# Kernel optimization log

Hardware: AMD Instinct MI355X
Metric: run time of the kernel (lower is better)

## Reference

```python
import jax, jax.numpy as jnp
import numpy as np
from jax import lax

KSIZE = 11
SIGMA = 1.5
C1 = (0.01 * 1.0) ** 2
C2 = (0.03 * 1.0) ** 2
PAD = (KSIZE - 1) // 2  # 5


def _gaussian_2d(ksize: int, sigma: float) -> np.ndarray:
    half = (ksize - 1) * 0.5
    g = np.exp(-0.5 * (np.linspace(-half, half, ksize) / sigma) ** 2)
    g = g / g.sum()
    return np.outer(g, g).astype(np.float32)  # [k, k]


def setup_inputs() -> dict:
    key = jax.random.key(0)
    kx, ky = jax.random.split(key)
    B, C, T, H, W = 2, 3, 8, 512, 512
    x = jax.random.uniform(kx, (B, C, T, H, W), dtype=jnp.float32)
    y = jax.random.uniform(ky, (B, C, T, H, W), dtype=jnp.float32)
    k2d = jnp.asarray(_gaussian_2d(KSIZE, SIGMA))
    # depthwise conv3d kernel: [C_out=C, C_in/groups=1, kD=1, kH, kW]
    kernel = jnp.broadcast_to(k2d[None, None, None], (C, 1, 1, KSIZE, KSIZE))
    return {"x": x, "y": y, "kernel": kernel}


def reference(x, y, kernel):
    C = x.shape[1]

    def conv(z):
        return lax.conv_general_dilated(
            z, kernel,
            window_strides=(1, 1, 1),
            padding=((0, 0), (PAD, PAD), (PAD, PAD)),
            dimension_numbers=("NCDHW", "OIDHW", "NCDHW"),
            feature_group_count=C,
        )

    # single grouped conv over the 5 stacked statistics, as in the original
    stacked = jnp.concatenate([x, y, x * x, y * y, x * y], axis=0)
    ux, uy, uxx, uyy, uxy = jnp.split(conv(stacked), 5, axis=0)

    vx = uxx - ux * ux
    vy = uyy - uy * uy
    vxy = uxy - ux * uy
    a1 = 2.0 * ux * uy + C1
    a2 = 2.0 * vxy + C2
    b1 = ux * ux + uy * uy + C1
    b2 = vx + vy + C2
    return a1 * a2 / (b1 * b2)
```

## Files before the change

### kernel.cpp

```cpp
#include <hip/hip_runtime.h>
#include <type_traits>

namespace {
constexpr int HH = 512;
constexpr int WW = 512;
constexpr int KS = 11;
constexpr int PADR = 5;
constexpr int TH = 32;
constexpr int TW = 64;
constexpr int HC = TW + 2 * PADR;
constexpr int LP = 76;
constexpr int NTHREADS = 256;
constexpr float SSIM_C1 = 1.0e-4f;
constexpr float SSIM_C2 = 9.0e-4f;
}

__global__ __launch_bounds__(NTHREADS, 3) void ssim_fused(
    const float* __restrict__ x, const float* __restrict__ y,
    const float* __restrict__ kern, float* __restrict__ out)
{
    __shared__ __align__(16) float vb[5][TH][LP];

    constexpr int tiles_w = WW / TW;
    constexpr int tiles_h = HH / TH;
    constexpr int tpp = tiles_w * tiles_h;

    const int bid = blockIdx.x;
    const int plane = bid / tpp;
    const int trem = bid - plane * tpp;
    const int tr_idx = trem / tiles_w;
    const int tile_r = tr_idx * TH;
    const int tile_c = (trem - tr_idx * tiles_w) * TW;

    const float* __restrict__ xp = x + (size_t)plane * (HH * WW);
    const float* __restrict__ yp = y + (size_t)plane * (HH * WW);
    float* __restrict__ op = out + (size_t)plane * (HH * WW);

    float wt[KS];
    {
        const float c = kern[5 * KS + 5];
        const float inv = rsqrtf(c);
#pragma unroll
        for (int i = 0; i < KS; ++i) wt[i] = kern[5 * KS + i] * inv;
    }

    const int t = threadIdx.x;
    const bool interior = (tile_r >= PADR) && (tile_r + TH + PADR <= HH) &&
                          (tile_c >= PADR) && (tile_c + TW + PADR <= WW);

    auto phase1 = [&](auto intr_tag) {
        constexpr bool INTR = decltype(intr_tag)::value;
        for (int i = t; i < TH * HC; i += NTHREADS) {
            const int r = i / HC;
            const int c = i - r * HC;
            const int gr = tile_r + r;
            const int gc = tile_c + c - PADR;
            float sx = 0.f, sy = 0.f, sxx = 0.f, syy = 0.f, sxy = 0.f;
            if (INTR) {
                const float* xq = xp + (size_t)(gr - PADR) * WW + gc;
                const float* yq = yp + (size_t)(gr - PADR) * WW + gc;
#pragma unroll
                for (int k = 0; k < KS; ++k) {
                    const float xv = xq[(size_t)k * WW];
                    const float yv = yq[(size_t)k * WW];
                    const float w = wt[k];
                    sx  += w * xv;
                    sy  += w * yv;
                    sxx += w * xv * xv;
                    syy += w * yv * yv;
                    sxy += w * xv * yv;
                }
            } else {
                const bool cok = (gc >= 0) & (gc < WW);
#pragma unroll
                for (int k = 0; k < KS; ++k) {
                    const int rr = gr - PADR + k;
                    const bool ok = cok & (rr >= 0) & (rr < HH);
                    float xv = 0.f, yv = 0.f;
                    if (ok) {
                        xv = xp[(size_t)rr * WW + gc];
                        yv = yp[(size_t)rr * WW + gc];
                    }
                    const float w = wt[k];
                    sx  += w * xv;
                    sy  += w * yv;
                    sxx += w * xv * xv;
                    syy += w * yv * yv;
                    sxy += w * xv * yv;
                }
            }
            vb[0][r][c] = sx;
            vb[1][r][c] = sy;
            vb[2][r][c] = sxx;
            vb[3][r][c] = syy;
            vb[4][r][c] = sxy;
        }
    };

    if (interior) phase1(std::true_type{});
    else          phase1(std::false_type{});

    __syncthreads();

#pragma unroll
    for (int gi = 0; gi < (TH * (TW / 4)) / NTHREADS; ++gi) {
        const int g = t + gi * NTHREADS;
        const int r = g >> 4;
        const int c0 = (g & 15) * 4;
        float res[5][4];
#pragma unroll
        for (int s = 0; s < 5; ++s) {
            float wnd[KS + 3];
#pragma unroll
            for (int i2 = 0; i2 < KS + 3; ++i2) wnd[i2] = vb[s][r][c0 + i2];
#pragma unroll
            for (int j = 0; j < 4; ++j) {
                float a = 0.f;
#pragma unroll
                for (int k = 0; k < KS; ++k) a += wt[k] * wnd[j + k];
                res[s][j] = a;
            }
        }
        float4 o;
#pragma unroll
        for (int j = 0; j < 4; ++j) {
            const float ux = res[0][j], uy = res[1][j];
            const float uxx = res[2][j], uyy = res[3][j], uxy = res[4][j];
            const float vx  = uxx - ux * ux;
            const float vy  = uyy - uy * uy;
            const float vxy = uxy - ux * uy;
            const float a1 = 2.f * ux * uy + SSIM_C1;
            const float a2 = 2.f * vxy + SSIM_C2;
            const float b1 = ux * ux + uy * uy + SSIM_C1;
            const float b2 = vx + vy + SSIM_C2;
            (&o.x)[j] = (a1 * a2) * __builtin_amdgcn_rcpf(b1 * b2);
        }
        *(float4*)(op + (size_t)(tile_r + r) * WW + (tile_c + c0)) = o;
    }
}

extern "C" void kernel_launch(void* const* d_in, const int* in_sizes, int n_in,
                              void* d_out, int out_size, void* d_ws, size_t ws_size,
                              hipStream_t stream) {
    const float* x    = (const float*)d_in[0];
    const float* y    = (const float*)d_in[1];
    const float* kern = (const float*)d_in[2];
    float* out = (float*)d_out;

    const int nplanes = in_sizes[0] / (HH * WW);
    const int nblocks = nplanes * (HH / TH) * (WW / TW);

    ssim_fused<<<dim3(nblocks), dim3(NTHREADS), 0, stream>>>(x, y, kern, out);
}
```

Measured before the change: 229.6 us.

## Restructure SSIM into full-width row bands with register-sliding vertical window

New measurement: 368.8 us. 60.6% more time.

```diff
diff --git a/kernel.cpp b/kernel.cpp
--- a/kernel.cpp
+++ b/kernel.cpp
@@ -1,36 +1,31 @@
 #include <hip/hip_runtime.h>
 #include <type_traits>
 
+typedef float v2f __attribute__((ext_vector_type(2)));
+
 namespace {
-constexpr int HH = 512;
-constexpr int WW = 512;
-constexpr int KS = 11;
-constexpr int PADR = 5;
-constexpr int TH = 32;
-constexpr int TW = 64;
-constexpr int HC = TW + 2 * PADR;
-constexpr int LP = 76;
-constexpr int NTHREADS = 256;
+constexpr int HH = 512, WW = 512;
+constexpr int KS = 11, PADR = 5;
+constexpr int BH = 32;
+constexpr int SR = 4;
+constexpr int NSLAB = BH / SR;
+constexpr int WIN = SR + 2*PADR;
+constexpr int PITCH = 528;
+constexpr int NT = 256;
 constexpr float SSIM_C1 = 1.0e-4f;
 constexpr float SSIM_C2 = 9.0e-4f;
 }
 
-__global__ __launch_bounds__(NTHREADS, 3) void ssim_fused(
+__global__ __launch_bounds__(NT, 3) void ssim_fused(
     const float* __restrict__ x, const float* __restrict__ y,
     const float* __restrict__ kern, float* __restrict__ out)
 {
-    __shared__ __align__(16) float vb[5][TH][LP];
-
-    constexpr int tiles_w = WW / TW;
-    constexpr int tiles_h = HH / TH;
-    constexpr int tpp = tiles_w * tiles_h;
+    __shared__ __align__(16) float vb[5][SR][PITCH];
 
     const int bid = blockIdx.x;
-    const int plane = bid / tpp;
-    const int trem = bid - plane * tpp;
-    const int tr_idx = trem / tiles_w;
-    const int tile_r = tr_idx * TH;
-    const int tile_c = (trem - tr_idx * tiles_w) * TW;
+    const int plane = bid >> 4;
+    const int band = bid & 15;
+    const int R0 = band << 5;
 
     const float* __restrict__ xp = x + (size_t)plane * (HH * WW);
     const float* __restrict__ yp = y + (size_t)plane * (HH * WW);
@@ -38,105 +33,157 @@
 
     float wt[KS];
     {
-        const float c = kern[5 * KS + 5];
-        const float inv = rsqrtf(c);
+        const float inv = rsqrtf(kern[5 * KS + 5]);
 #pragma unroll
         for (int i = 0; i < KS; ++i) wt[i] = kern[5 * KS + i] * inv;
     }
 
     const int t = threadIdx.x;
-    const bool interior = (tile_r >= PADR) && (tile_r + TH + PADR <= HH) &&
-                          (tile_c >= PADR) && (tile_c + TW + PADR <= WW);
-
-    auto phase1 = [&](auto intr_tag) {
-        constexpr bool INTR = decltype(intr_tag)::value;
-        for (int i = t; i < TH * HC; i += NTHREADS) {
-            const int r = i / HC;
-            const int c = i - r * HC;
-            const int gr = tile_r + r;
-            const int gc = tile_c + c - PADR;
-            float sx = 0.f, sy = 0.f, sxx = 0.f, syy = 0.f, sxy = 0.f;
-            if (INTR) {
-                const float* xq = xp + (size_t)(gr - PADR) * WW + gc;
-                const float* yq = yp + (size_t)(gr - PADR) * WW + gc;
-#pragma unroll
-                for (int k = 0; k < KS; ++k) {
-                    const float xv = xq[(size_t)k * WW];
-                    const float yv = yq[(size_t)k * WW];
-                    const float w = wt[k];
-                    sx  += w * xv;
-                    sy  += w * yv;
-                    sxx += w * xv * xv;
-                    syy += w * yv * yv;
-                    sxy += w * xv * yv;
-                }
-            } else {
-                const bool cok = (gc >= 0) & (gc < WW);
-#pragma unroll
-                for (int k = 0; k < KS; ++k) {
-                    const int rr = gr - PADR + k;
-                    const bool ok = cok & (rr >= 0) & (rr < HH);
-                    float xv = 0.f, yv = 0.f;
-                    if (ok) {
-                        xv = xp[(size_t)rr * WW + gc];
-                        yv = yp[(size_t)rr * WW + gc];
+    const int c2 = 2 * t;
+    const int q  = t & 127;
+    const int rb = (t >> 7) * 2;
+
+    for (int i = t; i < 5 * SR * 16; i += NT) {
+        const int st = i >> 6;
+        const int rem = i & 63;
+        const int r = rem >> 4;
+        const int j = rem & 15;
+        vb[st][r][(j < 8) ? j : (512 + j)] = 0.f;
+    }
+
+    auto body = [&](auto edge_tag) {
+        constexpr bool EDGE = decltype(edge_tag)::value;
+        const v2f zz = {0.f, 0.f};
+
+        auto ldrow = [&](int row, v2f& vx, v2f& vy) {
+            if (!EDGE || ((unsigned)row < (unsigned)HH)) {
+                vx = *(const v2f*)(xp + row * WW + c2);
+                vy = *(const v2f*)(yp + row * WW + c2);
+            } else { vx = zz; vy = zz; }
+        };
+
+        v2f xw[WIN], yw[WIN];
+#pragma unroll
+        for (int i = 0; i < WIN; ++i) ldrow(R0 - PADR + i, xw[i], yw[i]);
+
+        for (int s = 0; s < NSLAB; ++s) {
+#pragma unroll
+            for (int j = 0; j < SR; ++j) {
+                v2f a = wt[0] * xw[j];
+#pragma unroll
+                for (int k = 1; k < KS; ++k) a += wt[k] * xw[j + k];
+                *(v2f*)&vb[0][j][8 + c2] = a;
+            }
+#pragma unroll
+            for (int j = 0; j < SR; ++j) {
+                v2f a = wt[0] * yw[j];
+#pragma unroll
+                for (int k = 1; k < KS; ++k) a += wt[k] * yw[j + k];
+                *(v2f*)&vb[1][j][8 + c2] = a;
+            }
+            {
+                v2f tmp[WIN];
+#pragma unroll
+                for (int i = 0; i < WIN; ++i) tmp[i] = xw[i] * xw[i];
+#pragma unroll
+                for (int j = 0; j < SR; ++j) {
+                    v2f a = wt[0] * tmp[j];
+#pragma unroll
+                    for (int k = 1; k < KS; ++k) a += wt[k] * tmp[j + k];
+                    *(v2f*)&vb[2][j][8 + c2] = a;
+                }
+            }
+            {
+                v2f tmp[WIN];
+#pragma unroll
+                for (int i = 0; i < WIN; ++i) tmp[i] = yw[i] * yw[i];
+#pragma unroll
+                for (int j = 0; j < SR; ++j) {
+                    v2f a = wt[0] * tmp[j];
+#pragma unroll
+                    for (int k = 1; k < KS; ++k) a += wt[k] * tmp[j + k];
+                    *(v2f*)&vb[3][j][8 + c2] = a;
+                }
+            }
+            {
+                v2f tmp[WIN];
+#pragma unroll
+                for (int i = 0; i < WIN; ++i) tmp[i] = xw[i] * yw[i];
+#pragma unroll
+                for (int j = 0; j < SR; ++j) {
+                    v2f a = wt[0] * tmp[j];
+#pragma unroll
+                    for (int k = 1; k < KS; ++k) a += wt[k] * tmp[j + k];
+                    *(v2f*)&vb[4][j][8 + c2] = a;
+                }
+            }
+            __syncthreads();
+
+            v2f nx[SR], ny[SR];
+            if (s + 1 < NSLAB) {
+#pragma unroll
+                for (int j = 0; j < SR; ++j)
+                    ldrow(R0 - PADR + WIN + s * SR + j, nx[j], ny[j]);
+            }
+
+#pragma unroll
+            for (int rr = 0; rr < 2; ++rr) {
+                const int r = rb + rr;
+                float u[5][4];
+#pragma unroll
+                for (int st = 0; st < 5; ++st) {
+                    float wnd[20];
+#pragma unroll
+                    for (int ch = 0; ch < 5; ++ch) {
+                        const float4 v = *(const float4*)&vb[st][r][4 * q + 4 * ch];
+                        wnd[4 * ch + 0] = v.x;
+                        wnd[4 * ch + 1] = v.y;
+                        wnd[4 * ch + 2] = v.z;
+                        wnd[4 * ch + 3] = v.w;
                     }
-                    const float w = wt[k];
-                    sx  += w * xv;
-                    sy  += w * yv;
-                    sxx += w * xv * xv;
-                    syy += w * yv * yv;
-                    sxy += w * xv * yv;
-                }
-            }
-            vb[0][r][c] = sx;
-            vb[1][r][c] = sy;
-            vb[2][r][c] = sxx;
-            vb[3][r][c] = syy;
-            vb[4][r][c] = sxy;
+#pragma unroll
+                    for (int d = 0; d < 4; ++d) {
+                        float a = wt[0] * wnd[d + 3];
+#pragma unroll
+                        for (int k = 1; k < KS; ++k) a += wt[k] * wnd[d + 3 + k];
+                        u[st][d] = a;
+                    }
+                }
+                float4 o;
+#pragma unroll
+                for (int d = 0; d < 4; ++d) {
+                    const float ux = u[0][d], uy = u[1][d];
+                    const float uxx = u[2][d], uyy = u[3][d], uxy = u[4][d];
+                    const float vx  = uxx - ux * ux;
+                    const float vy  = uyy - uy * uy;
+                    const float vxy = uxy - ux * uy;
+                    const float a1 = 2.f * ux * uy + SSIM_C1;
+                    const float a2 = 2.f * vxy + SSIM_C2;
+                    const float b1 = ux * ux + uy * uy + SSIM_C1;
+                    const float b2 = vx + vy + SSIM_C2;
+                    (&o.x)[d] = (a1 * a2) * __builtin_amdgcn_rcpf(b1 * b2);
+                }
+                *(float4*)&op[(size_t)(R0 + s * SR + r) * WW + 4 * q] = o;
+            }
+            __syncthreads();
+
+            if (s + 1 < NSLAB) {
+#pragma unroll
+                for (int i = 0; i < WIN - SR; ++i) {
+                    xw[i] = xw[i + SR];
+                    yw[i] = yw[i + SR];
+                }
+#pragma unroll
+                for (int j = 0; j < SR; ++j) {
+                    xw[WIN - SR + j] = nx[j];
+                    yw[WIN - SR + j] = ny[j];
+                }
+            }
         }
     };
 
-    if (interior) phase1(std::true_type{});
-    else          phase1(std::false_type{});
-
-    __syncthreads();
-
-#pragma unroll
-    for (int gi = 0; gi < (TH * (TW / 4)) / NTHREADS; ++gi) {
-        const int g = t + gi * NTHREADS;
-        const int r = g >> 4;
-        const int c0 = (g & 15) * 4;
-        float res[5][4];
-#pragma unroll
-        for (int s = 0; s < 5; ++s) {
-            float wnd[KS + 3];
-#pragma unroll
-            for (int i2 = 0; i2 < KS + 3; ++i2) wnd[i2] = vb[s][r][c0 + i2];
-#pragma unroll
-            for (int j = 0; j < 4; ++j) {
-                float a = 0.f;
-#pragma unroll
-                for (int k = 0; k < KS; ++k) a += wt[k] * wnd[j + k];
-                res[s][j] = a;
-            }
-        }
-        float4 o;
-#pragma unroll
-        for (int j = 0; j < 4; ++j) {
-            const float ux = res[0][j], uy = res[1][j];
-            const float uxx = res[2][j], uyy = res[3][j], uxy = res[4][j];
-            const float vx  = uxx - ux * ux;
-            const float vy  = uyy - uy * uy;
-            const float vxy = uxy - ux * uy;
-            const float a1 = 2.f * ux * uy + SSIM_C1;
-            const float a2 = 2.f * vxy + SSIM_C2;
-            const float b1 = ux * ux + uy * uy + SSIM_C1;
-            const float b2 = vx + vy + SSIM_C2;
-            (&o.x)[j] = (a1 * a2) * __builtin_amdgcn_rcpf(b1 * b2);
-        }
-        *(float4*)(op + (size_t)(tile_r + r) * WW + (tile_c + c0)) = o;
-    }
+    if (band >= 1 && band <= 14) body(std::false_type{});
+    else                         body(std::true_type{});
 }
 
 extern "C" void kernel_launch(void* const* d_in, const int* in_sizes, int n_in,
@@ -148,7 +195,7 @@
     float* out = (float*)d_out;
 
     const int nplanes = in_sizes[0] / (HH * WW);
-    const int nblocks = nplanes * (HH / TH) * (WW / TW);
-
-    ssim_fused<<<dim3(nblocks), dim3(NTHREADS), 0, stream>>>(x, y, kern, out);
+    const int nblocks = nplanes * (HH / BH);
+
+    ssim_fused<<<dim3(nblocks), dim3(NT), 0, stream>>>(x, y, kern, out);
 }
```
